# Performance work log

Measured on AMD Instinct MI355X. Metric: run time of the kernel, lower is better.

## Reference

```python
import jax, jax.numpy as jnp
import numpy as np

N_NODES, N_EDGES, D_IN, N_GRAPHS = 20000, 320000, 256, 32
H1, C1, H2, C2 = 4, 128, 4, 64


def setup_inputs() -> dict:
    key = jax.random.key(0)
    ks = jax.random.split(key, 24)
    g = lambda k, shape, fan: jax.random.normal(k, shape, jnp.float32) * (1.0 / np.sqrt(fan))
    inp = {
        'x': jax.random.normal(ks[0], (N_NODES, D_IN), jnp.float32),
        'edge_index': jax.random.randint(ks[1], (2, N_EDGES), 0, N_NODES, jnp.int32),
        'batch': jnp.sort(jax.random.randint(ks[2], (N_NODES,), 0, N_GRAPHS, jnp.int32)),
        'edge_attr': jax.random.normal(ks[3], (N_EDGES, 1), jnp.float32),
        # GATConv 1: lin [D_IN, H1*C1], att_src/dst/edge [H1,C1], lin_edge [1,H1*C1], bias [H1*C1]
        'W1': g(ks[4], (D_IN, H1 * C1), D_IN),
        'as1': g(ks[5], (H1, C1), C1),
        'ad1': g(ks[6], (H1, C1), C1),
        'We1': g(ks[7], (1, H1 * C1), 1),
        'ae1': g(ks[8], (H1, C1), C1),
        'b1': jnp.zeros((H1 * C1,), jnp.float32),
        'g1': jnp.ones((H1 * C1,), jnp.float32),
        'be1': jnp.zeros((H1 * C1,), jnp.float32),
        # GATConv 2 (concat=False -> out 64)
        'W2': g(ks[9], (H1 * C1, H2 * C2), H1 * C1),
        'as2': g(ks[10], (H2, C2), C2),
        'ad2': g(ks[11], (H2, C2), C2),
        'We2': g(ks[12], (1, H2 * C2), 1),
        'ae2': g(ks[13], (H2, C2), C2),
        'b2': jnp.zeros((C2,), jnp.float32),
        'g2': jnp.ones((C2,), jnp.float32),
        'be2': jnp.zeros((C2,), jnp.float32),
        'fw1': g(ks[14], (C2, 32), C2),
        'fb1': jnp.zeros((32,), jnp.float32),
        'fw2': g(ks[15], (32, 1), 32),
        'fb2': jnp.zeros((1,), jnp.float32),
    }
    return inp


def _gat(x, src, dst, ea, W, a_s, a_d, We, a_e, bias, H, C, concat, n):
    h = (x @ W).reshape(n, H, C)                         # [N,H,C]
    al_s = jnp.einsum('nhc,hc->nh', h, a_s)              # [N,H]
    al_d = jnp.einsum('nhc,hc->nh', h, a_d)
    e = (ea @ We).reshape(-1, H, C)                      # [E',H,C]
    al_e = jnp.einsum('ehc,hc->eh', e, a_e)
    logits = jax.nn.leaky_relu(al_s[src] + al_d[dst] + al_e, 0.2)  # [E',H]
    m = jax.ops.segment_max(logits, dst, num_segments=n)
    m = jnp.where(jnp.isfinite(m), m, 0.0)
    p = jnp.exp(logits - m[dst])
    denom = jax.ops.segment_sum(p, dst, num_segments=n)
    alpha = p / (denom[dst] + 1e-16)                     # segment softmax
    out = jax.ops.segment_sum(h[src] * alpha[:, :, None], dst, num_segments=n)
    out = out.reshape(n, H * C) if concat else out.mean(axis=1)
    return out + bias


def _bn(x, gamma, beta):
    mu = x.mean(axis=0)
    var = x.var(axis=0)
    return gamma * (x - mu) * jax.lax.rsqrt(var + 1e-5) + beta


def reference(x, edge_index, batch, edge_attr, W1, as1, ad1, We1, ae1, b1, g1, be1,
              W2, as2, ad2, We2, ae2, b2, g2, be2, fw1, fb1, fw2, fb2):
    n = x.shape[0]
    loop = jnp.arange(n, dtype=edge_index.dtype)
    src = jnp.concatenate([edge_index[0], loop])
    dst = jnp.concatenate([edge_index[1], loop])
    # self-loop edge_attr filled with mean (PyG fill_value='mean')
    ea = jnp.concatenate([edge_attr, jnp.broadcast_to(edge_attr.mean(axis=0), (n, edge_attr.shape[1]))])

    h = _gat(x, src, dst, ea, W1, as1, ad1, We1, ae1, b1, H1, C1, True, n)
    h = jax.nn.elu(_bn(h, g1, be1))
    h = _gat(h, src, dst, ea, W2, as2, ad2, We2, ae2, b2, H2, C2, False, n)
    h = jax.nn.elu(_bn(h, g2, be2))

    sums = jax.ops.segment_sum(h, batch, num_segments=N_GRAPHS)
    cnt = jax.ops.segment_sum(jnp.ones((n,), h.dtype), batch, num_segments=N_GRAPHS)
    pooled = sums / jnp.maximum(cnt, 1.0)[:, None]       # global_mean_pool
    # dropout is identity in eval mode
    out = jax.nn.elu(pooled @ fw1 + fb1) @ fw2 + fb2
    return out
```

## Files before the change

### kernel.cpp

```cpp
#include <hip/hip_runtime.h>
#include <hip/hip_bf16.h>

#define N_NODES  20000
#define MPAD     20096
#define N_EDGES  320000
#define N_EP     (N_EDGES + N_NODES)
#define D_IN     256
#define N_GRAPHS 32
#define HH1 4
#define CC1 128
#define HH2 4
#define CC2 64
#define MAXDEG   128

#define XB_OFF      0ull
#define HB1_OFF     10289152ull
#define AGG1_OFF    30867456ull
#define HB2_OFF     51445760ull
#define OUT2_OFF    61734912ull
#define EAF_OFF     66854912ull
#define W1BT_OFF    68134912ull
#define W2BT_OFF    68397056ull
#define CSR_OFF     68659200ull
#define ROWPTR_OFF  71379200ull
#define GSTART_OFF  71459264ull
#define SMALL_OFF   71459520ull
#define SBUF_OFF    71485120ull
#define EAP_OFF     71485184ull
#define PMU1_OFF    72772608ull
#define PM21_OFF    73296896ull
#define PMU2_OFF    73821184ull
#define PM22_OFF    73886720ull
#define A1_OFF      73952256ull
#define B1_OFF      73954304ull
#define A2_OFF      73956352ull
#define B2_OFF      73956608ull
#define EAACC_OFF   73956864ull
#define DEG_OFF     74600000ull
#define CURS_OFF    74680000ull
#define FLAGZ_OFF   74760000ull
#define PP_OFF      74760128ull
#define ALS1_OFF    74825664ull
#define ALD1_OFF    75147200ull
#define ALS2_OFF    75468736ull
#define ALD2_OFF    75790272ull
#define ZERO0_START DEG_OFF
#define ZERO0_SIZE  1511808ull

#define S_AS1 0
#define S_AD1 512
#define S_WE1 1024
#define S_AE1 1536
#define S_G1  2048
#define S_BE1 2560
#define S_AS2 3072
#define S_AD2 3328
#define S_WE2 3584
#define S_AE2 3840
#define S_G2  4096
#define S_BE2 4160
#define S_FW1 4224
#define S_FB1 6272
#define S_FW2 6304
#define S_FB2 6336

typedef __attribute__((ext_vector_type(8))) short bf8_t;
typedef __attribute__((ext_vector_type(4))) float f4_t;

__global__ void detect_dtype(const unsigned short* __restrict__ xr, int* __restrict__ flag) {
    int i = blockIdx.x * blockDim.x + threadIdx.x;
    unsigned short u = xr[i];
    if ((u & 0x7F80) == 0x7F80) atomicOr(flag, 1);
}

__device__ __forceinline__ float loadF(const void* p, int i, int fp32) {
    return fp32 ? ((const float*)p)[i]
                : __bfloat162float(((const __hip_bfloat16*)p)[i]);
}

#define PB_XB  5024
#define PB_EAF 313
#define PB_W   512
#define PB_SM  16
#define PREP_BLOCKS (PB_XB + PB_EAF + 2 * PB_W + PB_SM + 1)
__global__ __launch_bounds__(256) void prep(
        const int* __restrict__ flag,
        const void* x, const void* ea, const void* W1, const void* W2,
        const void* as1, const void* ad1, const void* We1, const void* ae1,
        const void* g1, const void* be1, const void* as2, const void* ad2,
        const void* We2, const void* ae2, const void* g2, const void* be2,
        const void* fw1, const void* fb1, const void* fw2, const void* fb2,
        __hip_bfloat16* __restrict__ xb, float* __restrict__ eaf, float* __restrict__ eap,
        __hip_bfloat16* __restrict__ W1bt, __hip_bfloat16* __restrict__ W2bt,
        float* __restrict__ smalls, float* __restrict__ sbuf) {
    __shared__ float sh[256];
    int b = blockIdx.x, t = threadIdx.x;
    int fp32 = flag[0];
    if (b < PB_XB) {
        int base = (b * 256 + t) * 4;
        __hip_bfloat16 tmp[4];
#pragma unroll
        for (int j = 0; j < 4; ++j) {
            int i = base + j;
            float v = (i < N_NODES * D_IN) ? loadF(x, i, fp32) : 0.f;
            tmp[j] = __float2bfloat16(v);
        }
        *(uint2*)&xb[base] = *(uint2*)tmp;
        return;
    }
    b -= PB_XB;
    if (b < PB_EAF) {
        int base = (b * 256 + t) * 4;
        float s = 0.f;
#pragma unroll
        for (int j = 0; j < 4; ++j) {
            int i = base + j;
            if (i < N_EDGES) { float v = loadF(ea, i, fp32); eaf[i] = v; s += v; }
        }
        sh[t] = s;
        __syncthreads();
        for (int st = 128; st; st >>= 1) {
            if (t < st) sh[t] += sh[t + st];
            __syncthreads();
        }
        if (t == 0) eap[b] = sh[0];
        return;
    }
    b -= PB_EAF;
    if (b < PB_W) {
        int i = b * 256 + t;
        int k = i >> 9, n = i & 511;
        W1bt[(size_t)n * 256 + k] = __float2bfloat16(loadF(W1, i, fp32));
        return;
    }
    b -= PB_W;
    if (b < PB_W) {
        int i = b * 256 + t;
        int k = i >> 8, n = i & 255;
        W2bt[(size_t)n * 512 + k] = __float2bfloat16(loadF(W2, i, fp32));
        return;
    }
    b -= PB_W;
    if (b < PB_SM) {
        const void* srcs[16] = {as1, ad1, We1, ae1, g1, be1, as2, ad2, We2, ae2, g2, be2, fw1, fb1, fw2, fb2};
        const int cnts[16] = {512, 512, 512, 512, 512, 512, 256, 256, 256, 256, 64, 64, 2048, 32, 32, 1};
        const int offs[16] = {S_AS1, S_AD1, S_WE1, S_AE1, S_G1, S_BE1, S_AS2, S_AD2,
                              S_WE2, S_AE2, S_G2, S_BE2, S_FW1, S_FB1, S_FW2, S_FB2};
        for (int i = t; i < cnts[b]; i += 256)
            smalls[offs[b] + i] = loadF(srcs[b], i, fp32);
        return;
    }
    if (t < 4) {
        float s = 0.f;
        for (int c = 0; c < CC1; ++c) s += loadF(We1, t * CC1 + c, fp32) * loadF(ae1, t * CC1 + c, fp32);
        sbuf[t] = s;
    } else if (t < 8) {
        int h = t - 4;
        float s = 0.f;
        for (int c = 0; c < CC2; ++c) s += loadF(We2, h * CC2 + c, fp32) * loadF(ae2, h * CC2 + c, fp32);
        sbuf[4 + h] = s;
    }
}

#define HIST_BLOCKS 1329
__global__ void hist_bounds(const int* __restrict__ ei, int* __restrict__ deg,
                            const int* __restrict__ batch, int* __restrict__ gstart) {
    int b = blockIdx.x, t = threadIdx.x;
    if (b < HIST_BLOCKS) {
        int e = b * 256 + t;
        if (e >= N_EP) return;
        int d = (e < N_EDGES) ? ei[N_EDGES + e] : e - N_EDGES;
        atomicAdd(&deg[d], 1);
        return;
    }
    int i = (b - HIST_BLOCKS) * 256 + t;
    if (i >= N_NODES) return;
    int bb = batch[i];
    if (i == 0) {
        for (int g = 0; g <= bb; ++g) gstart[g] = 0;
    } else {
        int pb = batch[i - 1];
        for (int g = pb + 1; g <= bb; ++g) gstart[g] = i;
    }
    if (i == N_NODES - 1) {
        for (int g = bb + 1; g <= N_GRAPHS; ++g) gstart[g] = N_NODES;
    }
}

__global__ __launch_bounds__(1024) void deg_scan(const int* __restrict__ deg, int* __restrict__ rowptr,
                                                 const float* __restrict__ eap, float* __restrict__ ea_acc) {
    __shared__ int part[1024];
    __shared__ float fsh[512];
    int t = threadIdx.x;
    int lo = t * 20;
    int hi = lo + 20; if (hi > N_NODES) hi = N_NODES; if (lo > N_NODES) lo = N_NODES;
    int s = 0;
    for (int i = lo; i < hi; ++i) s += deg[i];
    part[t] = s;
    __syncthreads();
    for (int off = 1; off < 1024; off <<= 1) {
        int u = (t >= off) ? part[t - off] : 0;
        __syncthreads();
        if (t >= off) part[t] += u;
        __syncthreads();
    }
    int run = part[t] - s;
    for (int i = lo; i < hi; ++i) { rowptr[i] = run; run += deg[i]; }
    if (hi == N_NODES && lo < N_NODES) rowptr[N_NODES] = run;
    if (t < 512) fsh[t] = (t < PB_EAF) ? eap[t] : 0.f;
    __syncthreads();
    for (int st = 256; st; st >>= 1) {
        if (t < st) fsh[t] += fsh[t + st];
        __syncthreads();
    }
    if (t == 0) ea_acc[0] = fsh[0];
}

__global__ void edge_scatter(const int* __restrict__ ei, const int* __restrict__ rowptr,
                             int* __restrict__ cursor, int2* __restrict__ csr_se) {
    int e = blockIdx.x * blockDim.x + threadIdx.x;
    if (e >= N_EP) return;
    int s, d;
    if (e < N_EDGES) { s = ei[e]; d = ei[N_EDGES + e]; }
    else { s = d = e - N_EDGES; }
    int pos = rowptr[d] + atomicAdd(&cursor[d], 1);
    csr_se[pos] = make_int2(s, e);
}

__global__ __launch_bounds__(64) void csr_sort_fill(const int* __restrict__ rowptr, int2* __restrict__ cs,
                                                    const float* __restrict__ eaf,
                                                    const float* __restrict__ ea_acc) {
    __shared__ int2 buf[128];
    int d = blockIdx.x;
    int beg = rowptr[d], end = rowptr[d + 1], n = end - beg;
    int lane = threadIdx.x;
    float ea_mean = ea_acc[0] * (1.0f / N_EDGES);
    if (n <= 0) return;
    if (n <= 128) {
        for (int i = lane; i < n; i += 64) buf[i] = cs[beg + i];
        __syncthreads();
        for (int r = 0; r < n; ++r) {
            int i = 2 * lane + (r & 1);
            if (i + 1 < n) {
                int2 a = buf[i], b = buf[i + 1];
                if (a.y > b.y) { buf[i] = b; buf[i + 1] = a; }
            }
            __syncthreads();
        }
        for (int i = lane; i < n; i += 64) {
            int2 se = buf[i];
            float eav = (se.y < N_EDGES) ? eaf[se.y] : ea_mean;
            se.y = __float_as_int(eav);
            cs[beg + i] = se;
        }
    } else {
        if (lane == 0) {
            for (int i = beg + 1; i < end; ++i) {
                int2 key = cs[i]; int j = i - 1;
                while (j >= beg && cs[j].y > key.y) { cs[j + 1] = cs[j]; --j; }
                cs[j + 1] = key;
            }
        }
        __syncthreads();
        for (int i = lane; i < n; i += 64) {
            int2 se = cs[beg + i];
            float eav = (se.y < N_EDGES) ? eaf[se.y] : ea_mean;
            se.y = __float_as_int(eav);
            cs[beg + i] = se;
        }
    }
}

__global__ __launch_bounds__(256) void gemm_mfma_al(
        const short* __restrict__ A, const short* __restrict__ Bt,
        __hip_bfloat16* __restrict__ Cb, int N, int K,
        float* __restrict__ als, float* __restrict__ ald,
        const float* __restrict__ asv, const float* __restrict__ adv, int cshift) {
    __shared__ short As[128 * 40];
    __shared__ short Bs[64 * 40];
    int t = threadIdx.x;
    int wv = t >> 6, lane = t & 63, quad = lane >> 4, lr = lane & 15;
    int m0 = blockIdx.y * 128, n0 = blockIdx.x * 64;
    f4_t acc[2][4] = {};
    int ra0 = t >> 2, sa0 = t & 3;
    int ra1 = (t + 256) >> 2;
    for (int k0 = 0; k0 < K; k0 += 32) {
        *(uint4*)&As[ra0 * 40 + sa0 * 8] = *(const uint4*)&A[(size_t)(m0 + ra0) * K + k0 + sa0 * 8];
        *(uint4*)&As[ra1 * 40 + sa0 * 8] = *(const uint4*)&A[(size_t)(m0 + ra1) * K + k0 + sa0 * 8];
        *(uint4*)&Bs[ra0 * 40 + sa0 * 8] = *(const uint4*)&Bt[(size_t)(n0 + ra0) * K + k0 + sa0 * 8];
        __syncthreads();
        bf8_t a0 = *(const bf8_t*)&As[(wv * 16 + lr) * 40 + quad * 8];
        bf8_t a1 = *(const bf8_t*)&As[((wv + 4) * 16 + lr) * 40 + quad * 8];
#pragma unroll
        for (int nt = 0; nt < 4; ++nt) {
            bf8_t b = *(const bf8_t*)&Bs[(nt * 16 + lr) * 40 + quad * 8];
            acc[0][nt] = __builtin_amdgcn_mfma_f32_16x16x32_bf16(a0, b, acc[0][nt], 0, 0, 0);
            acc[1][nt] = __builtin_amdgcn_mfma_f32_16x16x32_bf16(a1, b, acc[1][nt], 0, 0, 0);
        }
        __syncthreads();
    }
#pragma unroll
    for (int si = 0; si < 2; ++si) {
        int mrow = m0 + (wv + si * 4) * 16 + quad * 4;
#pragma unroll
        for (int nt = 0; nt < 4; ++nt) {
            int col = n0 + nt * 16 + lr;
#pragma unroll
            for (int r = 0; r < 4; ++r)
                Cb[(size_t)(mrow + r) * N + col] = __float2bfloat16(acc[si][nt][r]);
        }
    }
    float asv4[4], adv4[4];
#pragma unroll
    for (int nt = 0; nt < 4; ++nt) {
        asv4[nt] = asv[n0 + nt * 16 + lr];
        adv4[nt] = adv[n0 + nt * 16 + lr];
    }
    int hsel = n0 >> cshift;
#pragma unroll
    for (int si = 0; si < 2; ++si) {
#pragma unroll
        for (int r = 0; r < 4; ++r) {
            float ps = 0.f, pd = 0.f;
#pragma unroll
            for (int nt = 0; nt < 4; ++nt) {
                ps += acc[si][nt][r] * asv4[nt];
                pd += acc[si][nt][r] * adv4[nt];
            }
#pragma unroll
            for (int m = 1; m < 16; m <<= 1) {
                ps += __shfl_xor(ps, m);
                pd += __shfl_xor(pd, m);
            }
            if (lr == 0) {
                int row = m0 + (wv + si * 4) * 16 + quad * 4 + r;
                atomicAdd(&als[row * 4 + hsel], ps);
                atomicAdd(&ald[row * 4 + hsel], pd);
            }
        }
    }
}

__global__ __launch_bounds__(256) void fused_agg1(
        const int* __restrict__ rowptr, const int2* __restrict__ cs,
        const float* __restrict__ als, const float* __restrict__ ald,
        const float* __restrict__ sbuf, const __hip_bfloat16* __restrict__ hb,
        __hip_bfloat16* __restrict__ outb) {
    __shared__ float lg[4][MAXDEG * 4];
    __shared__ int   ssrc[4][MAXDEG];
    int wv = threadIdx.x >> 6, t = threadIdx.x & 63;
    int d = blockIdx.x * 4 + wv;
    int beg = rowptr[d], n = rowptr[d + 1] - beg;
    bool fit = (n <= MAXDEG);
    float4 adv = *(const float4*)&ald[d * 4];
    float adh[4] = {adv.x, adv.y, adv.z, adv.w};
    float sb4[4] = {sbuf[0], sbuf[1], sbuf[2], sbuf[3]};
    float mx[4] = {-INFINITY, -INFINITY, -INFINITY, -INFINITY};
    for (int p = t; p < n; p += 64) {
        int2 se = cs[beg + p];
        float eav = __int_as_float(se.y);
        float4 as = *(const float4*)&als[se.x * 4];
        float l[4] = {as.x, as.y, as.z, as.w};
#pragma unroll
        for (int hh = 0; hh < 4; ++hh) {
            float v = l[hh] + adh[hh] + eav * sb4[hh];
            v = v > 0.f ? v : 0.2f * v;
            l[hh] = v;
            mx[hh] = fmaxf(mx[hh], v);
        }
        if (fit) {
            *(float4*)&lg[wv][p * 4] = make_float4(l[0], l[1], l[2], l[3]);
            ssrc[wv][p] = se.x;
        }
    }
#pragma unroll
    for (int m = 1; m < 64; m <<= 1)
#pragma unroll
        for (int hh = 0; hh < 4; ++hh)
            mx[hh] = fmaxf(mx[hh], __shfl_xor(mx[hh], m));
    asm volatile("s_waitcnt lgkmcnt(0)" ::: "memory");
    int h = t >> 4;
    float mh = mx[h];
    float a[8] = {};
    float ds = 0.f;
    const __hip_bfloat16* hrow = hb + 8 * t;
#define ACC8(rr, wt) { \
    unsigned q0 = (rr).x, q1 = (rr).y, q2 = (rr).z, q3 = (rr).w; \
    a[0] += (wt) * __uint_as_float(q0 << 16); a[1] += (wt) * __uint_as_float(q0 & 0xFFFF0000u); \
    a[2] += (wt) * __uint_as_float(q1 << 16); a[3] += (wt) * __uint_as_float(q1 & 0xFFFF0000u); \
    a[4] += (wt) * __uint_as_float(q2 << 16); a[5] += (wt) * __uint_as_float(q2 & 0xFFFF0000u); \
    a[6] += (wt) * __uint_as_float(q3 << 16); a[7] += (wt) * __uint_as_float(q3 & 0xFFFF0000u); }
    if (fit) {
        int p = 0;
        for (; p + 8 <= n; p += 8) {
            int s0 = ssrc[wv][p],     s1 = ssrc[wv][p + 1], s2 = ssrc[wv][p + 2], s3 = ssrc[wv][p + 3];
            int s4 = ssrc[wv][p + 4], s5 = ssrc[wv][p + 5], s6 = ssrc[wv][p + 6], s7 = ssrc[wv][p + 7];
            uint4 r0 = *(const uint4*)&hrow[(size_t)s0 * 512];
            uint4 r1 = *(const uint4*)&hrow[(size_t)s1 * 512];
            uint4 r2 = *(const uint4*)&hrow[(size_t)s2 * 512];
            uint4 r3 = *(const uint4*)&hrow[(size_t)s3 * 512];
            uint4 r4 = *(const uint4*)&hrow[(size_t)s4 * 512];
            uint4 r5 = *(const uint4*)&hrow[(size_t)s5 * 512];
            uint4 r6 = *(const uint4*)&hrow[(size_t)s6 * 512];
            uint4 r7 = *(const uint4*)&hrow[(size_t)s7 * 512];
            float w0 = __expf(lg[wv][p * 4 + h] - mh);
            float w1 = __expf(lg[wv][p * 4 + 4 + h] - mh);
            float w2 = __expf(lg[wv][p * 4 + 8 + h] - mh);
            float w3 = __expf(lg[wv][p * 4 + 12 + h] - mh);
            float w4 = __expf(lg[wv][p * 4 + 16 + h] - mh);
            float w5 = __expf(lg[wv][p * 4 + 20 + h] - mh);
            float w6 = __expf(lg[wv][p * 4 + 24 + h] - mh);
            float w7 = __expf(lg[wv][p * 4 + 28 + h] - mh);
            ds += ((w0 + w1) + (w2 + w3)) + ((w4 + w5) + (w6 + w7));
            ACC8(r0, w0); ACC8(r1, w1); ACC8(r2, w2); ACC8(r3, w3);
            ACC8(r4, w4); ACC8(r5, w5); ACC8(r6, w6); ACC8(r7, w7);
        }
        for (; p + 4 <= n; p += 4) {
            int s0 = ssrc[wv][p], s1 = ssrc[wv][p + 1], s2 = ssrc[wv][p + 2], s3 = ssrc[wv][p + 3];
            uint4 r0 = *(const uint4*)&hrow[(size_t)s0 * 512];
            uint4 r1 = *(const uint4*)&hrow[(size_t)s1 * 512];
            uint4 r2 = *(const uint4*)&hrow[(size_t)s2 * 512];
            uint4 r3 = *(const uint4*)&hrow[(size_t)s3 * 512];
            float w0 = __expf(lg[wv][p * 4 + h] - mh);
            float w1 = __expf(lg[wv][p * 4 + 4 + h] - mh);
            float w2 = __expf(lg[wv][p * 4 + 8 + h] - mh);
            float w3 = __expf(lg[wv][p * 4 + 12 + h] - mh);
            ds += (w0 + w1) + (w2 + w3);
            ACC8(r0, w0); ACC8(r1, w1); ACC8(r2, w2); ACC8(r3, w3);
        }
        for (; p < n; ++p) {
            int s0 = ssrc[wv][p];
            uint4 r0 = *(const uint4*)&hrow[(size_t)s0 * 512];
            float w0 = __expf(lg[wv][p * 4 + h] - mh);
            ds += w0;
            ACC8(r0, w0);
        }
    } else {
        for (int p = 0; p < n; ++p) {
            int2 se = cs[beg + p];
            float eav = __int_as_float(se.y);
            float l = als[se.x * 4 + h] + adh[h] + eav * sb4[h];
            l = l > 0.f ? l : 0.2f * l;
            float w = __expf(l - mh);
            uint4 r0 = *(const uint4*)&hrow[(size_t)se.x * 512];
            ds += w;
            ACC8(r0, w);
        }
    }
#undef ACC8
    float rdn = 1.0f / (ds + 1e-16f);
    __hip_bfloat16 tmp[8];
#pragma unroll
    for (int j = 0; j < 8; ++j) tmp[j] = __float2bfloat16(a[j] * rdn);
    *(uint4*)&outb[(size_t)d * 512 + 8 * t] = *(uint4*)tmp;
}

__global__ __launch_bounds__(256) void fused_agg2(
        const int* __restrict__ rowptr, const int2* __restrict__ cs,
        const float* __restrict__ als, const float* __restrict__ ald,
        const float* __restrict__ sbuf, const __hip_bfloat16* __restrict__ hb,
        float* __restrict__ out2) {
    __shared__ float lg[4][MAXDEG * 4];
    __shared__ int   ssrc[4][MAXDEG];
    int wv = threadIdx.x >> 6, t = threadIdx.x & 63;
    int d = blockIdx.x * 4 + wv;
    int beg = rowptr[d], n = rowptr[d + 1] - beg;
    bool fit = (n <= MAXDEG);
    float4 adv = *(const float4*)&ald[d * 4];
    float adh[4] = {adv.x, adv.y, adv.z, adv.w};
    float sb4[4] = {sbuf[4], sbuf[5], sbuf[6], sbuf[7]};
    float mx[4] = {-INFINITY, -INFINITY, -INFINITY, -INFINITY};
    for (int p = t; p < n; p += 64) {
        int2 se = cs[beg + p];
        float eav = __int_as_float(se.y);
        float4 as = *(const float4*)&als[se.x * 4];
        float l[4] = {as.x, as.y, as.z, as.w};
#pragma unroll
        for (int hh = 0; hh < 4; ++hh) {
            float v = l[hh] + adh[hh] + eav * sb4[hh];
            v = v > 0.f ? v : 0.2f * v;
            l[hh] = v;
            mx[hh] = fmaxf(mx[hh], v);
        }
        if (fit) {
            *(float4*)&lg[wv][p * 4] = make_float4(l[0], l[1], l[2], l[3]);
            ssrc[wv][p] = se.x;
        }
    }
#pragma unroll
    for (int m = 1; m < 64; m <<= 1)
#pragma unroll
        for (int hh = 0; hh < 4; ++hh)
            mx[hh] = fmaxf(mx[hh], __shfl_xor(mx[hh], m));
    asm volatile("s_waitcnt lgkmcnt(0)" ::: "memory");
    int h = t >> 4;
    float mh = mx[h];
    float a4[4] = {};
    float ds = 0.f;
    const __hip_bfloat16* hrow = hb + 4 * t;
#define ACC4(rr, wt) { \
    unsigned q0 = (rr).x, q1 = (rr).y; \
    a4[0] += (wt) * __uint_as_float(q0 << 16); a4[1] += (wt) * __uint_as_float(q0 & 0xFFFF0000u); \
    a4[2] += (wt) * __uint_as_float(q1 << 16); a4[3] += (wt) * __uint_as_float(q1 & 0xFFFF0000u); }
    if (fit) {
        int p = 0;
        for (; p + 8 <= n; p += 8) {
            int s0 = ssrc[wv][p],     s1 = ssrc[wv][p + 1], s2 = ssrc[wv][p + 2], s3 = ssrc[wv][p + 3];
            int s4 = ssrc[wv][p + 4], s5 = ssrc[wv][p + 5], s6 = ssrc[wv][p + 6], s7 = ssrc[wv][p + 7];
            uint2 r0 = *(const uint2*)&hrow[(size_t)s0 * 256];
            uint2 r1 = *(const uint2*)&hrow[(size_t)s1 * 256];
            uint2 r2 = *(const uint2*)&hrow[(size_t)s2 * 256];
            uint2 r3 = *(const uint2*)&hrow[(size_t)s3 * 256];
            uint2 r4 = *(const uint2*)&hrow[(size_t)s4 * 256];
            uint2 r5 = *(const uint2*)&hrow[(size_t)s5 * 256];
            uint2 r6 = *(const uint2*)&hrow[(size_t)s6 * 256];
            uint2 r7 = *(const uint2*)&hrow[(size_t)s7 * 256];
            float w0 = __expf(lg[wv][p * 4 + h] - mh);
            float w1 = __expf(lg[wv][p * 4 + 4 + h] - mh);
            float w2 = __expf(lg[wv][p * 4 + 8 + h] - mh);
            float w3 = __expf(lg[wv][p * 4 + 12 + h] - mh);
            float w4 = __expf(lg[wv][p * 4 + 16 + h] - mh);
            float w5 = __expf(lg[wv][p * 4 + 20 + h] - mh);
            float w6 = __expf(lg[wv][p * 4 + 24 + h] - mh);
            float w7 = __expf(lg[wv][p * 4 + 28 + h] - mh);
            ds += ((w0 + w1) + (w2 + w3)) + ((w4 + w5) + (w6 + w7));
            ACC4(r0, w0); ACC4(r1, w1); ACC4(r2, w2); ACC4(r3, w3);
            ACC4(r4, w4); ACC4(r5, w5); ACC4(r6, w6); ACC4(r7, w7);
        }
        for (; p + 4 <= n; p += 4) {
            int s0 = ssrc[wv][p], s1 = ssrc[wv][p + 1], s2 = ssrc[wv][p + 2], s3 = ssrc[wv][p + 3];
            uint2 r0 = *(const uint2*)&hrow[(size_t)s0 * 256];
            uint2 r1 = *(const uint2*)&hrow[(size_t)s1 * 256];
            uint2 r2 = *(const uint2*)&hrow[(size_t)s2 * 256];
            uint2 r3 = *(const uint2*)&hrow[(size_t)s3 * 256];
            float w0 = __expf(lg[wv][p * 4 + h] - mh);
            float w1 = __expf(lg[wv][p * 4 + 4 + h] - mh);
            float w2 = __expf(lg[wv][p * 4 + 8 + h] - mh);
            float w3 = __expf(lg[wv][p * 4 + 12 + h] - mh);
            ds += (w0 + w1) + (w2 + w3);
            ACC4(r0, w0); ACC4(r1, w1); ACC4(r2, w2); ACC4(r3, w3);
        }
        for (; p < n; ++p) {
            int s0 = ssrc[wv][p];
            uint2 r0 = *(const uint2*)&hrow[(size_t)s0 * 256];
            float w0 = __expf(lg[wv][p * 4 + h] - mh);
            ds += w0;
            ACC4(r0, w0);
        }
    } else {
        for (int p = 0; p < n; ++p) {
            int2 se = cs[beg + p];
            float eav = __int_as_float(se.y);
            float l = als[se.x * 4 + h] + adh[h] + eav * sb4[h];
            l = l > 0.f ? l : 0.2f * l;
            float w = __expf(l - mh);
            uint2 r0 = *(const uint2*)&hrow[(size_t)se.x * 256];
            ds += w;
            ACC4(r0, w);
        }
    }
#undef ACC4
    float rdn = 1.0f / (ds + 1e-16f);
#pragma unroll
    for (int j = 0; j < 4; ++j) {
        float v = a4[j] * rdn;
        v += __shfl_xor(v, 16);
        v += __shfl_xor(v, 32);
        a4[j] = v * 0.25f;
    }
    if (t < 16)
        *(float4*)&out2[(size_t)d * 64 + 4 * t] = make_float4(a4[0], a4[1], a4[2], a4[3]);
}

__global__ __launch_bounds__(256) void bn_part_b(const __hip_bfloat16* __restrict__ x,
                                                 float* __restrict__ pmu, float* __restrict__ pm2) {
    int t = threadIdx.x, b = blockIdx.x;
    float s0 = 0.f, s20 = 0.f, s1 = 0.f, s21 = 0.f;
    for (int i = b; i < N_NODES; i += gridDim.x) {
        unsigned u = *(const unsigned*)&x[(size_t)i * 512 + 2 * t];
        float v0 = __uint_as_float(u << 16);
        float v1 = __uint_as_float(u & 0xFFFF0000u);
        s0 += v0; s20 += v0 * v0; s1 += v1; s21 += v1 * v1;
    }
    pmu[b * 512 + 2 * t] = s0;     pm2[b * 512 + 2 * t] = s20;
    pmu[b * 512 + 2 * t + 1] = s1; pm2[b * 512 + 2 * t + 1] = s21;
}

__global__ void bn_reduce_affine(const float* __restrict__ pmu, const float* __restrict__ pm2,
                                 const float* __restrict__ smalls, int s_g, int s_be,
                                 float* __restrict__ a, float* __restrict__ b, int nch) {
    int c = blockIdx.x * blockDim.x + threadIdx.x;
    if (c >= nch) return;
    float s = 0.f, s2 = 0.f;
    for (int bk = 0; bk < 256; ++bk) { s += pmu[bk * nch + c]; s2 += pm2[bk * nch + c]; }
    float m = s * (1.0f / N_NODES);
    float var = s2 * (1.0f / N_NODES) - m * m;
    float aa = smalls[s_g + c] * rsqrtf(var + 1e-5f);
    a[c] = aa;
    b[c] = smalls[s_be + c] - m * aa;
}

__global__ __launch_bounds__(256) void bn_apply_elu_b16(__hip_bfloat16* __restrict__ x,
                                                        const float* __restrict__ a,
                                                        const float* __restrict__ b) {
    int q = blockIdx.x * blockDim.x + threadIdx.x;
    if (q >= N_NODES * 512 / 4) return;
    int base = q * 4;
    int j = base & 511;
    uint2 raw = *(uint2*)&x[base];
    float v[4] = {__uint_as_float(raw.x << 16), __uint_as_float(raw.x & 0xFFFF0000u),
                  __uint_as_float(raw.y << 16), __uint_as_float(raw.y & 0xFFFF0000u)};
    __hip_bfloat16 tmp[4];
#pragma unroll
    for (int k = 0; k < 4; ++k) {
        float y = a[j + k] * v[k] + b[j + k];
        y = y > 0.f ? y : expm1f(y);
        tmp[k] = __float2bfloat16(y);
    }
    *(uint2*)&x[base] = *(uint2*)tmp;
}

__global__ __launch_bounds__(256) void bn2_stats(const float* __restrict__ x,
                                                 float* __restrict__ pmu, float* __restrict__ pm2) {
    int t = threadIdx.x;
    int c = t & 63, j = t >> 6;
    float ls = 0.f, ls2 = 0.f;
    for (int nd = blockIdx.x * 4 + j; nd < N_NODES; nd += gridDim.x * 4) {
        float v = x[(size_t)nd * 64 + c];
        ls += v; ls2 += v * v;
    }
    __shared__ float shs[4][64], sh2[4][64];
    shs[j][c] = ls; sh2[j][c] = ls2;
    __syncthreads();
    if (j == 0) {
        pmu[blockIdx.x * 64 + c] = shs[0][c] + shs[1][c] + shs[2][c] + shs[3][c];
        pm2[blockIdx.x * 64 + c] = sh2[0][c] + sh2[1][c] + sh2[2][c] + sh2[3][c];
    }
}

__global__ __launch_bounds__(256) void pool_mlp(const float* __restrict__ x, const int* __restrict__ gstart,
                                                const float* __restrict__ a2, const float* __restrict__ b2,
                                                const float* __restrict__ smalls, const int* __restrict__ flag,
                                                void* __restrict__ outp) {
    int g = blockIdx.x, t = threadIdx.x;
    int c = t & 63, j = t >> 6;
    int beg = gstart[g], end = gstart[g + 1];
    float ac = a2[c], bc = b2[c];
    float s = 0.f;
    for (int i = beg + j; i < end; i += 4) {
        float y = ac * x[(size_t)i * 64 + c] + bc;
        s += (y > 0.f ? y : expm1f(y));
    }
    __shared__ float sh[4][64];
    __shared__ float pooled[64];
    __shared__ float hsh[32];
    sh[j][c] = s;
    __syncthreads();
    if (t < 64) {
        int n = end - beg;
        pooled[t] = (sh[0][t] + sh[1][t] + sh[2][t] + sh[3][t]) / fmaxf((float)n, 1.0f);
    }
    __syncthreads();
    if (t < 32) {
        float acc = smalls[S_FB1 + t];
        for (int cc = 0; cc < 64; ++cc)
            acc += pooled[cc] * smalls[S_FW1 + cc * 32 + t];
        hsh[t] = acc > 0.f ? acc : expm1f(acc);
    }
    __syncthreads();
    if (t == 0) {
        float o = smalls[S_FB2];
        for (int k = 0; k < 32; ++k) o += hsh[k] * smalls[S_FW2 + k];
        if (flag[0]) ((float*)outp)[g] = o;
        else ((__hip_bfloat16*)outp)[g] = __float2bfloat16(o);
    }
}

extern "C" void kernel_launch(void* const* d_in, const int* in_sizes, int n_in,
                              void* d_out, int out_size, void* d_ws, size_t ws_size,
                              hipStream_t stream) {
    const void* x    = d_in[0];
    const int* ei    = (const int*)d_in[1];
    const int* batch = (const int*)d_in[2];
    const void* ea   = d_in[3];
    const void* W1   = d_in[4];
    const void* as1  = d_in[5];
    const void* ad1  = d_in[6];
    const void* We1  = d_in[7];
    const void* ae1  = d_in[8];
    const void* g1   = d_in[10];
    const void* be1  = d_in[11];
    const void* W2   = d_in[12];
    const void* as2  = d_in[13];
    const void* ad2  = d_in[14];
    const void* We2  = d_in[15];
    const void* ae2  = d_in[16];
    const void* g2   = d_in[18];
    const void* be2  = d_in[19];
    const void* fw1  = d_in[20];
    const void* fb1  = d_in[21];
    const void* fw2  = d_in[22];
    const void* fb2  = d_in[23];

    char* ws = (char*)d_ws;
    __hip_bfloat16* xb   = (__hip_bfloat16*)(ws + XB_OFF);
    __hip_bfloat16* hb1  = (__hip_bfloat16*)(ws + HB1_OFF);
    __hip_bfloat16* agg1 = (__hip_bfloat16*)(ws + AGG1_OFF);
    __hip_bfloat16* hb2  = (__hip_bfloat16*)(ws + HB2_OFF);
    float* out2   = (float*)(ws + OUT2_OFF);
    float* eaf    = (float*)(ws + EAF_OFF);
    __hip_bfloat16* W1bt = (__hip_bfloat16*)(ws + W1BT_OFF);
    __hip_bfloat16* W2bt = (__hip_bfloat16*)(ws + W2BT_OFF);
    int2*  csr_se = (int2*)(ws + CSR_OFF);
    int*   rowptr = (int*)(ws + ROWPTR_OFF);
    int*   gstart = (int*)(ws + GSTART_OFF);
    float* smalls = (float*)(ws + SMALL_OFF);
    float* sbuf   = (float*)(ws + SBUF_OFF);
    float* eap    = (float*)(ws + EAP_OFF);
    float* pmu1   = (float*)(ws + PMU1_OFF);
    float* pm21   = (float*)(ws + PM21_OFF);
    float* pmu2   = (float*)(ws + PMU2_OFF);
    float* pm22   = (float*)(ws + PM22_OFF);
    float* a1     = (float*)(ws + A1_OFF);
    float* b1     = (float*)(ws + B1_OFF);
    float* a2     = (float*)(ws + A2_OFF);
    float* b2     = (float*)(ws + B2_OFF);
    float* ea_acc = (float*)(ws + EAACC_OFF);
    float* als1   = (float*)(ws + ALS1_OFF);
    float* ald1   = (float*)(ws + ALD1_OFF);
    float* als2   = (float*)(ws + ALS2_OFF);
    float* ald2   = (float*)(ws + ALD2_OFF);
    int*   deg    = (int*)(ws + DEG_OFF);
    int*   cursor = (int*)(ws + CURS_OFF);
    int*   flag   = (int*)(ws + FLAGZ_OFF);

    hipMemsetAsync(ws + ZERO0_START, 0, ZERO0_SIZE, stream);

    detect_dtype<<<256, 256, 0, stream>>>((const unsigned short*)x, flag);
    prep<<<PREP_BLOCKS, 256, 0, stream>>>(flag, x, ea, W1, W2,
                                          as1, ad1, We1, ae1, g1, be1, as2, ad2,
                                          We2, ae2, g2, be2, fw1, fb1, fw2, fb2,
                                          xb, eaf, eap, W1bt, W2bt, smalls, sbuf);

    hist_bounds<<<HIST_BLOCKS + 79, 256, 0, stream>>>(ei, deg, batch, gstart);
    deg_scan<<<1, 1024, 0, stream>>>(deg, rowptr, eap, ea_acc);
    edge_scatter<<<HIST_BLOCKS, 256, 0, stream>>>(ei, rowptr, cursor, csr_se);
    csr_sort_fill<<<N_NODES, 64, 0, stream>>>(rowptr, csr_se, eaf, ea_acc);

    gemm_mfma_al<<<dim3(512 / 64, MPAD / 128), 256, 0, stream>>>(
        (const short*)xb, (const short*)W1bt, hb1, 512, 256,
        als1, ald1, smalls + S_AS1, smalls + S_AD1, 7);
    fused_agg1<<<N_NODES / 4, 256, 0, stream>>>(rowptr, csr_se, als1, ald1, sbuf, hb1, agg1);
    bn_part_b<<<256, 256, 0, stream>>>(agg1, pmu1, pm21);
    bn_reduce_affine<<<2, 256, 0, stream>>>(pmu1, pm21, smalls, S_G1, S_BE1, a1, b1, 512);
    bn_apply_elu_b16<<<10000, 256, 0, stream>>>(agg1, a1, b1);

    gemm_mfma_al<<<dim3(256 / 64, MPAD / 128), 256, 0, stream>>>(
        (const short*)agg1, (const short*)W2bt, hb2, 256, 512,
        als2, ald2, smalls + S_AS2, smalls + S_AD2, 6);
    fused_agg2<<<N_NODES / 4, 256, 0, stream>>>(rowptr, csr_se, als2, ald2, sbuf, hb2, out2);
    bn2_stats<<<256, 256, 0, stream>>>(out2, pmu2, pm22);
    bn_reduce_affine<<<1, 64, 0, stream>>>(pmu2, pm22, smalls, S_G2, S_BE2, a2, b2, 64);

    pool_mlp<<<N_GRAPHS, 256, 0, stream>>>(out2, gstart, a2, b2, smalls, flag, d_out);
}
```

Before: 477.5 us.

## Parallelize CSR sorting per wave and split pooling across more blocks

Rows of up to 64 edges are now sorted with a register-resident odd-even transposition sort using wave shuffles. Each 256-thread block handles four destination nodes, one per wave, and `__syncthreads` becomes a wave-local waitcnt. Mean pooling is split into 8 chunks per graph feeding a small finishing kernel that runs the MLP, which raises parallelism over the 32-block version. The edge-attribute block reduction also switches to wave shuffles. The trade-offs are a fixed 64-round sort even for low-degree rows and one extra kernel launch.

```diff
diff --git a/kernel.cpp b/kernel.cpp
--- a/kernel.cpp
+++ b/kernel.cpp
@@ -93,7 +93,7 @@
         __hip_bfloat16* __restrict__ xb, float* __restrict__ eaf, float* __restrict__ eap,
         __hip_bfloat16* __restrict__ W1bt, __hip_bfloat16* __restrict__ W2bt,
         float* __restrict__ smalls, float* __restrict__ sbuf) {
-    __shared__ float sh[256];
+    __shared__ float shw[4];
     int b = blockIdx.x, t = threadIdx.x;
     int fp32 = flag[0];
     if (b < PB_XB) {
@@ -117,13 +117,11 @@
             int i = base + j;
             if (i < N_EDGES) { float v = loadF(ea, i, fp32); eaf[i] = v; s += v; }
         }
-        sh[t] = s;
+#pragma unroll
+        for (int m = 1; m < 64; m <<= 1) s += __shfl_xor(s, m);
+        if ((t & 63) == 0) shw[t >> 6] = s;
         __syncthreads();
-        for (int st = 128; st; st >>= 1) {
-            if (t < st) sh[t] += sh[t + st];
-            __syncthreads();
-        }
-        if (t == 0) eap[b] = sh[0];
+        if (t == 0) eap[b] = shw[0] + shw[1] + shw[2] + shw[3];
         return;
     }
     b -= PB_EAF;
@@ -227,47 +225,67 @@
     csr_se[pos] = make_int2(s, e);
 }
 
-__global__ __launch_bounds__(64) void csr_sort_fill(const int* __restrict__ rowptr, int2* __restrict__ cs,
-                                                    const float* __restrict__ eaf,
-                                                    const float* __restrict__ ea_acc) {
-    __shared__ int2 buf[128];
-    int d = blockIdx.x;
+__global__ __launch_bounds__(256) void csr_sort_fill(const int* __restrict__ rowptr, int2* __restrict__ cs,
+                                                     const float* __restrict__ eaf,
+                                                     const float* __restrict__ ea_acc) {
+    __shared__ int2 buf[4][128];
+    int wv = threadIdx.x >> 6, lane = threadIdx.x & 63;
+    int d = blockIdx.x * 4 + wv;
     int beg = rowptr[d], end = rowptr[d + 1], n = end - beg;
-    int lane = threadIdx.x;
     float ea_mean = ea_acc[0] * (1.0f / N_EDGES);
     if (n <= 0) return;
+    if (n <= 64) {
+        int key = 0x7FFFFFFF, val = 0;
+        if (lane < n) { int2 se = cs[beg + lane]; key = se.y; val = se.x; }
+        for (int r = 0; r < 64; ++r) {
+            int par = r & 1;
+            bool up = ((lane & 1) == par);
+            int partner = up ? lane + 1 : lane - 1;
+            bool valid = (partner >= 0) && (partner < 64);
+            int pidx = valid ? partner : lane;
+            int pk = __shfl(key, pidx);
+            int pv = __shfl(val, pidx);
+            bool take = valid && (up ? (pk < key) : (pk > key));
+            if (take) { key = pk; val = pv; }
+        }
+        if (lane < n) {
+            float eav = (key < N_EDGES) ? eaf[key] : ea_mean;
+            cs[beg + lane] = make_int2(val, __float_as_int(eav));
+        }
+        return;
+    }
     if (n <= 128) {
-        for (int i = lane; i < n; i += 64) buf[i] = cs[beg + i];
-        __syncthreads();
+        for (int i = lane; i < n; i += 64) buf[wv][i] = cs[beg + i];
+        asm volatile("s_waitcnt lgkmcnt(0)" ::: "memory");
         for (int r = 0; r < n; ++r) {
             int i = 2 * lane + (r & 1);
             if (i + 1 < n) {
-                int2 a = buf[i], b = buf[i + 1];
-                if (a.y > b.y) { buf[i] = b; buf[i + 1] = a; }
+                int2 a = buf[wv][i], b = buf[wv][i + 1];
+                if (a.y > b.y) { buf[wv][i] = b; buf[wv][i + 1] = a; }
             }
-            __syncthreads();
+            asm volatile("s_waitcnt lgkmcnt(0)" ::: "memory");
         }
         for (int i = lane; i < n; i += 64) {
-            int2 se = buf[i];
+            int2 se = buf[wv][i];
             float eav = (se.y < N_EDGES) ? eaf[se.y] : ea_mean;
             se.y = __float_as_int(eav);
             cs[beg + i] = se;
         }
-    } else {
-        if (lane == 0) {
-            for (int i = beg + 1; i < end; ++i) {
-                int2 key = cs[i]; int j = i - 1;
-                while (j >= beg && cs[j].y > key.y) { cs[j + 1] = cs[j]; --j; }
-                cs[j + 1] = key;
-            }
-        }
-        __syncthreads();
-        for (int i = lane; i < n; i += 64) {
-            int2 se = cs[beg + i];
-            float eav = (se.y < N_EDGES) ? eaf[se.y] : ea_mean;
-            se.y = __float_as_int(eav);
-            cs[beg + i] = se;
-        }
+        return;
+    }
+    if (lane == 0) {
+        for (int i = beg + 1; i < end; ++i) {
+            int2 key = cs[i]; int j = i - 1;
+            while (j >= beg && cs[j].y > key.y) { cs[j + 1] = cs[j]; --j; }
+            cs[j + 1] = key;
+        }
+    }
+    asm volatile("s_waitcnt vmcnt(0)" ::: "memory");
+    for (int i = lane; i < n; i += 64) {
+        int2 se = cs[beg + i];
+        float eav = (se.y < N_EDGES) ? eaf[se.y] : ea_mean;
+        se.y = __float_as_int(eav);
+        cs[beg + i] = se;
     }
 }
 
@@ -638,28 +656,37 @@
     }
 }
 
-__global__ __launch_bounds__(256) void pool_mlp(const float* __restrict__ x, const int* __restrict__ gstart,
-                                                const float* __restrict__ a2, const float* __restrict__ b2,
-                                                const float* __restrict__ smalls, const int* __restrict__ flag,
-                                                void* __restrict__ outp) {
-    int g = blockIdx.x, t = threadIdx.x;
+__global__ __launch_bounds__(256) void pool_part(const float* __restrict__ x, const int* __restrict__ gstart,
+                                                 const float* __restrict__ a2, const float* __restrict__ b2,
+                                                 float* __restrict__ pp) {
+    int g = blockIdx.x >> 3, ck = blockIdx.x & 7;
+    int t = threadIdx.x;
     int c = t & 63, j = t >> 6;
-    int beg = gstart[g], end = gstart[g + 1];
+    int beg = gstart[g], end = gstart[g + 1], n = end - beg;
+    int cb = beg + (n * ck) / 8, ce = beg + (n * (ck + 1)) / 8;
     float ac = a2[c], bc = b2[c];
     float s = 0.f;
-    for (int i = beg + j; i < end; i += 4) {
+    for (int i = cb + j; i < ce; i += 4) {
         float y = ac * x[(size_t)i * 64 + c] + bc;
         s += (y > 0.f ? y : expm1f(y));
     }
     __shared__ float sh[4][64];
+    sh[j][c] = s;
+    __syncthreads();
+    if (j == 0)
+        pp[blockIdx.x * 64 + c] = sh[0][c] + sh[1][c] + sh[2][c] + sh[3][c];
+}
+
+__global__ __launch_bounds__(64) void pool_mlp_fin(const float* __restrict__ pp, const int* __restrict__ gstart,
+                                                   const float* __restrict__ smalls, const int* __restrict__ flag,
+                                                   void* __restrict__ outp) {
+    int g = blockIdx.x, t = threadIdx.x;
     __shared__ float pooled[64];
     __shared__ float hsh[32];
-    sh[j][c] = s;
-    __syncthreads();
-    if (t < 64) {
-        int n = end - beg;
-        pooled[t] = (sh[0][t] + sh[1][t] + sh[2][t] + sh[3][t]) / fmaxf((float)n, 1.0f);
-    }
+    float s = 0.f;
+    for (int k = 0; k < 8; ++k) s += pp[(g * 8 + k) * 64 + t];
+    int n = gstart[g + 1] - gstart[g];
+    pooled[t] = s / fmaxf((float)n, 1.0f);
     __syncthreads();
     if (t < 32) {
         float acc = smalls[S_FB1 + t];
@@ -730,6 +757,7 @@
     float* ald1   = (float*)(ws + ALD1_OFF);
     float* als2   = (float*)(ws + ALS2_OFF);
     float* ald2   = (float*)(ws + ALD2_OFF);
+    float* pp     = (float*)(ws + PP_OFF);
     int*   deg    = (int*)(ws + DEG_OFF);
     int*   cursor = (int*)(ws + CURS_OFF);
     int*   flag   = (int*)(ws + FLAGZ_OFF);
@@ -745,7 +773,7 @@
     hist_bounds<<<HIST_BLOCKS + 79, 256, 0, stream>>>(ei, deg, batch, gstart);
     deg_scan<<<1, 1024, 0, stream>>>(deg, rowptr, eap, ea_acc);
     edge_scatter<<<HIST_BLOCKS, 256, 0, stream>>>(ei, rowptr, cursor, csr_se);
-    csr_sort_fill<<<N_NODES, 64, 0, stream>>>(rowptr, csr_se, eaf, ea_acc);
+    csr_sort_fill<<<N_NODES / 4, 256, 0, stream>>>(rowptr, csr_se, eaf, ea_acc);
 
     gemm_mfma_al<<<dim3(512 / 64, MPAD / 128), 256, 0, stream>>>(
         (const short*)xb, (const short*)W1bt, hb1, 512, 256,
@@ -762,5 +790,6 @@
     bn2_stats<<<256, 256, 0, stream>>>(out2, pmu2, pm22);
     bn_reduce_affine<<<1, 64, 0, stream>>>(pmu2, pm22, smalls, S_G2, S_BE2, a2, b2, 64);
 
-    pool_mlp<<<N_GRAPHS, 256, 0, stream>>>(out2, gstart, a2, b2, smalls, flag, d_out);
-}
+    pool_part<<<N_GRAPHS * 8, 256, 0, stream>>>(out2, gstart, a2, b2, pp);
+    pool_mlp_fin<<<N_GRAPHS, 64, 0, stream>>>(pp, gstart, smalls, flag, d_out);
+}
```

After: 444.6 us. -6.9%, faster.
